# Kernel optimization log

Measured on AMD Instinct MI355X. Metric: run time of the kernel, lower is better.

## Reference

```python
import jax, jax.numpy as jnp
import numpy as np

B, L, G, P, K = 16, 2048, 8, 8, 64
CLAMP = 15.0


def _cdist(x, y):
    # Euclidean pairwise distance: x [..., K, 3], y [..., L, 3] -> [..., K, L]
    x2 = jnp.sum(x * x, axis=-1)[..., :, None]
    y2 = jnp.sum(y * y, axis=-1)[..., None, :]
    xy = jnp.einsum('...kc,...lc->...kl', x, y)
    return jnp.sqrt(jnp.maximum(x2 + y2 - 2.0 * xy, 0.0))


def setup_inputs() -> dict:
    key = jax.random.key(0)
    k1, k2, k3 = jax.random.split(key, 3)
    rng = np.random.default_rng(0)
    # each group: K distinct atom indices; each of the P rows is a permutation of them
    auto = np.empty((G, P, K), dtype=np.int64)
    for g in range(G):
        base = rng.permutation(L)[:K]
        auto[g, 0] = base
        for j in range(1, P):
            auto[g, j] = base[rng.permutation(K)]
    return {
        'x_pred': jax.random.normal(k1, (B, L, 3), jnp.float32),
        'x_native': jax.random.normal(k2, (B, L, 3), jnp.float32),
        'x_native_mask': jax.random.randint(k3, (B, L), 0, 2).astype(bool),
        'automorphs': jnp.asarray(auto),
    }


def reference(x_pred, x_native, x_native_mask, automorphs):
    Bn, Ln = x_pred.shape[0], x_pred.shape[1]
    Kn = automorphs.shape[-1]
    batch_idx = jnp.arange(Bn)
    denom = jnp.asarray(Kn * (Ln - Kn), x_pred.dtype)

    def step(carry, a):
        x_nat, nat_mask = carry
        a0 = a[0]                                           # [K]
        # columns NOT in the symmetry group (the ~mask columns)
        colmask = jnp.ones((Ln,), x_pred.dtype).at[a0].set(0.0)
        d_pred = _cdist(x_pred[:, a0], x_pred)              # [B,K,L]
        gath = x_nat[:, a]                                  # [B,P,K,3]
        d_nat = _cdist(gath, x_nat[:, None])                # [B,P,K,L]
        drms = jnp.minimum(jnp.nan_to_num(jnp.square(d_pred[:, None] - d_nat)), CLAMP)
        drms = jnp.sum(drms * colmask, axis=(-1, -2)) / denom   # [B,P] masked mean
        bestj = jnp.argmin(drms, axis=1)                    # first min <=> strict-< update
        sel = gath[batch_idx, bestj]                        # [B,K,3]
        sel_m = nat_mask[:, a][batch_idx, bestj]            # [B,K]
        x_nat = x_nat.at[:, a0].set(sel)
        nat_mask = nat_mask.at[:, a0].set(sel_m)
        return (x_nat, nat_mask), None

    (x_nat, nat_mask), _ = jax.lax.scan(step, (x_native, x_native_mask), automorphs)
    return x_nat, nat_mask
```

## Files before the change

kernel.cpp:

```cpp
#include <hip/hip_runtime.h>
#include <math.h>

#define Bn 16
#define Ln 2048
#define Gn 8
#define Pn 8
#define Kn 64
#define CLAMP_V 15.0f

#define BPB 32
#define NTH 512
#define NWV (NTH / 64)
#define LPB (Ln / BPB)
#define LPW (LPB / NWV)
#define PK  (Pn * Kn)

#define MAGIC(g) (0x5EED0000u | (unsigned)(g))

typedef unsigned long long ull;

__device__ __forceinline__ float wave_sum64(float x) {
#define DPP_ADD(ctrl) \
    x += __int_as_float(__builtin_amdgcn_update_dpp(0, __float_as_int(x), ctrl, 0xf, 0xf, true))
    DPP_ADD(0x111);
    DPP_ADD(0x112);
    DPP_ADD(0x114);
    DPP_ADD(0x118);
    DPP_ADD(0x142);
    DPP_ADD(0x143);
#undef DPP_ADD
    return x;
}

template <int IMM>
__device__ __forceinline__ float swz_xor(float v) {
    return v + __int_as_float(__builtin_amdgcn_ds_swizzle(__float_as_int(v), IMM));
}
__device__ __forceinline__ ull ld_rlx64(const ull* p) {
    return __hip_atomic_load(p, __ATOMIC_RELAXED, __HIP_MEMORY_SCOPE_AGENT);
}
__device__ __forceinline__ void st_rlx64(ull* p, ull v) {
    __hip_atomic_store(p, v, __ATOMIC_RELAXED, __HIP_MEMORY_SCOPE_AGENT);
}

__global__ __launch_bounds__(NTH, 2) void fused_kernel(
    const float* __restrict__ xpred, const float* __restrict__ xnat,
    const int* __restrict__ mask_in, const int* __restrict__ autom,
    float* __restrict__ out_x, float* __restrict__ out_m,
    ull* __restrict__ part) {

    const int tid  = threadIdx.x;
    const int lane = tid & 63;
    const int wv   = tid >> 6;
    const int b    = blockIdx.x >> 5;
    const int c    = blockIdx.x & (BPB - 1);

    __shared__ float4         s_all[Ln];
    __shared__ unsigned short s_idx[Ln];
    __shared__ unsigned char  s_inv[2][Ln];
    __shared__ float4         s_xp[LPB];
    __shared__ float          s_part[NWV][Pn];

    const float* xpb = xpred + (size_t)b * Ln * 3;
    const float* xnb = xnat  + (size_t)b * Ln * 3;

    for (int l = tid; l < Ln; l += NTH) {
        s_idx[l] = (unsigned short)l;
        s_all[l] = make_float4(xnb[l * 3 + 0], xnb[l * 3 + 1], xnb[l * 3 + 2], 0.0f);
    }
    if (wv == 0) {
        const int l = c * LPB + lane;
        s_xp[lane] = make_float4(xpb[l * 3 + 0], xpb[l * 3 + 1], xpb[l * 3 + 2], 0.0f);
    } else if (wv == 2) {
        s_inv[0][autom[lane]] = (unsigned char)lane;
    }
    int   a0k = autom[lane];
    float px = xpb[a0k * 3 + 0], py = xpb[a0k * 3 + 1], pz = xpb[a0k * 3 + 2];
    __syncthreads();

    #pragma unroll 1
    for (int g = 0; g < Gn; g++) {
        const int* ag  = autom + g * PK;
        const int* ag1 = autom + (g + 1) * PK;
        const int  cur = g & 1, nxt = cur ^ 1;
        ull* pg = part + (size_t)(g * Bn + b) * (BPB * Pn);

        const float4 nk = s_all[s_idx[a0k]];
        int sig[Pn];
        #pragma unroll
        for (int p = 0; p < Pn; p++)
            sig[p] = 4 * (int)s_inv[cur][ag[p * Kn + lane]];
        unsigned short jl[LPW];
        #pragma unroll
        for (int i = 0; i < LPW; i++)
            jl[i] = s_idx[c * LPB + wv * LPW + i];

        float acc[Pn];
        #pragma unroll
        for (int p = 0; p < Pn; p++) acc[p] = 0.0f;

        #pragma unroll 2
        for (int i = 0; i < LPW; i++) {
            const int il = wv * LPW + i;
            const int l  = c * LPB + il;
            if (__ballot(a0k == l)) continue;

            const float4 q = s_xp[il];
            const float4 m = s_all[jl[i]];
            const float dx = px - q.x, dy = py - q.y, dz = pz - q.z;
            const float dp = __builtin_amdgcn_sqrtf(dx * dx + dy * dy + dz * dz);
            const float ex = nk.x - m.x, ey = nk.y - m.y, ez = nk.z - m.z;
            const float dn = __builtin_amdgcn_sqrtf(ex * ex + ey * ey + ez * ez);

            #pragma unroll
            for (int p = 0; p < Pn; p++) {
                const float dns = __int_as_float(
                    __builtin_amdgcn_ds_bpermute(sig[p], __float_as_int(dn)));
                const float e = dp - dns;
                acc[p] += fminf(e * e, CLAMP_V);
            }
        }

        #pragma unroll
        for (int p = 0; p < Pn; p++) {
            const float v = wave_sum64(acc[p]);
            if (lane == 63) s_part[wv][p] = v;
        }
        __syncthreads();

        if (wv == 0) {
            float v = s_part[lane >> 3][lane & 7];
            v = swz_xor<0x201F>(v);
            v = swz_xor<0x401F>(v);
            v += __shfl(v, lane + 32, 64);
            if (lane < 8)
                st_rlx64(&pg[c * Pn + lane],
                         ((ull)MAGIC(g) << 32) | (ull)__float_as_uint(v));
        }

        if (g < Gn - 1) {
            a0k = ag1[lane];
            px = xpb[a0k * 3 + 0]; py = xpb[a0k * 3 + 1]; pz = xpb[a0k * 3 + 2];
            if (wv == 2) s_inv[nxt][ag1[lane]] = (unsigned char)lane;
        }

        if (wv == 0) {
            const unsigned magic = MAGIC(g);
            ull q0 = 0, q1 = 0, q2 = 0, q3 = 0;
            bool r0 = false, r1 = false, r2 = false, r3 = false;
            for (;;) {
                if (!r0) { q0 = ld_rlx64(pg + lane);       r0 = (unsigned)(q0 >> 32) == magic; }
                if (!r1) { q1 = ld_rlx64(pg + lane + 64);  r1 = (unsigned)(q1 >> 32) == magic; }
                if (!r2) { q2 = ld_rlx64(pg + lane + 128); r2 = (unsigned)(q2 >> 32) == magic; }
                if (!r3) { q3 = ld_rlx64(pg + lane + 192); r3 = (unsigned)(q3 >> 32) == magic; }
                if (__ballot(!(r0 && r1 && r2 && r3)) == 0ull) break;
                __builtin_amdgcn_s_sleep(1);
            }
            float v = __uint_as_float((unsigned)q0) + __uint_as_float((unsigned)q1)
                    + __uint_as_float((unsigned)q2) + __uint_as_float((unsigned)q3);
            v = swz_xor<0x201F>(v);
            v = swz_xor<0x401F>(v);
            v += __shfl(v, lane + 32, 64);
            float best = __shfl(v, 0, 64);
            int   bj   = 0;
            #pragma unroll
            for (int p = 1; p < Pn; p++) {
                const float t = __shfl(v, p, 64);
                if (t < best) { best = t; bj = p; }
            }
            const unsigned short oldv = s_idx[ag[bj * Kn + lane]];
            s_idx[ag[lane]] = oldv;
        }
        __syncthreads();
    }

    const int l0 = c * LPB;
    if (tid < LPB * 3) {
        const int ll = tid / 3, coord = tid % 3;
        const int l  = l0 + ll;
        const float4 v = s_all[s_idx[l]];
        out_x[((size_t)b * Ln + l) * 3 + coord] =
            (coord == 0) ? v.x : ((coord == 1) ? v.y : v.z);
    } else if (tid < LPB * 4) {
        const int l = l0 + (tid - LPB * 3);
        const int j = s_idx[l];
        out_m[(size_t)b * Ln + l] = (float)mask_in[(size_t)b * Ln + j];
    }
}

extern "C" void kernel_launch(void* const* d_in, const int* in_sizes, int n_in,
                              void* d_out, int out_size, void* d_ws, size_t ws_size,
                              hipStream_t stream) {
    const float* xpred   = (const float*)d_in[0];
    const float* xnat_in = (const float*)d_in[1];
    const int*   mask_in = (const int*)  d_in[2];
    const int*   autom   = (const int*)  d_in[3];

    float* out_x = (float*)d_out;
    float* out_m = out_x + Bn * Ln * 3;

    ull* part = (ull*)d_ws;

    fused_kernel<<<Bn * BPB, NTH, 0, stream>>>(
        xpred, xnat_in, mask_in, autom, out_x, out_m, part);
}
```

Measured before the change: 116.1 us.

## Speculatively compute next group's distances before cross-block argmin resolves

Computes the next group's masked distance sums before the grid-wide argmin for the current group has been resolved, so the dependent work overlaps the spin-wait on partial sums. Columns and rows whose native coordinates the pending update may change are skipped, then fixed up afterwards. The fix-up covers overlapping group columns and anchor atoms altered by the previous step. It also reformulates the permutation so the predicted distance is permuted via ds_permute-derived indices instead of the native one. This adds substantial complexity, extra LDS state and syncs, and a correctness risk if the speculation bookkeeping is wrong.

Result: slower. 126.3 us (+8.8%).

```diff
diff --git a/kernel.cpp b/kernel.cpp
--- a/kernel.cpp
+++ b/kernel.cpp
@@ -58,8 +58,10 @@
     __shared__ float4         s_all[Ln];
     __shared__ unsigned short s_idx[Ln];
     __shared__ unsigned char  s_inv[2][Ln];
+    __shared__ unsigned char  s_stp[2][Ln];
     __shared__ float4         s_xp[LPB];
     __shared__ float          s_part[NWV][Pn];
+    __shared__ float          s_par2[2][NWV][Pn];
 
     const float* xpb = xpred + (size_t)b * Ln * 3;
     const float* xnb = xnat  + (size_t)b * Ln * 3;
@@ -67,69 +69,103 @@
     for (int l = tid; l < Ln; l += NTH) {
         s_idx[l] = (unsigned short)l;
         s_all[l] = make_float4(xnb[l * 3 + 0], xnb[l * 3 + 1], xnb[l * 3 + 2], 0.0f);
-    }
+        s_stp[0][l] = 0xFF;
+        s_stp[1][l] = 0xFF;
+    }
+    __syncthreads();
+
     if (wv == 0) {
         const int l = c * LPB + lane;
         s_xp[lane] = make_float4(xpb[l * 3 + 0], xpb[l * 3 + 1], xpb[l * 3 + 2], 0.0f);
     } else if (wv == 2) {
         s_inv[0][autom[lane]] = (unsigned char)lane;
-    }
-    int   a0k = autom[lane];
-    float px = xpb[a0k * 3 + 0], py = xpb[a0k * 3 + 1], pz = xpb[a0k * 3 + 2];
+    } else if (wv == 3) {
+        s_stp[0][autom[lane]] = 0;
+    }
+    if (lane < Pn) s_par2[0][wv][lane] = 0.0f;
+
+    int   a0n = autom[lane];
+    int   a0c = a0n;
+    float pxn = xpb[a0n * 3 + 0], pyn = xpb[a0n * 3 + 1], pzn = xpb[a0n * 3 + 2];
     __syncthreads();
+
+    int            sigf[Pn];
+    unsigned short jlv[LPW];
+    float          nsx, nsy, nsz;
+    unsigned       m8n = 0, mg8n = 0;
+    float          acc[Pn];
+    bool           skipme = false;
+
+    auto body = [&](int il, float ncx, float ncy, float ncz, int jidx) {
+        const float4 q = s_xp[il];
+        const float4 m = s_all[jidx];
+        const float2 ux = make_float2(pxn - q.x, ncx - m.x);
+        const float2 uy = make_float2(pyn - q.y, ncy - m.y);
+        const float2 uz = make_float2(pzn - q.z, ncz - m.z);
+        const float2 ss = ux * ux + uy * uy + uz * uz;
+        const float dp = __builtin_amdgcn_sqrtf(ss.x);
+        const float dn = __builtin_amdgcn_sqrtf(ss.y);
+        const int dpi = __float_as_int(dp);
+        const float e0 = dp - dn;
+        acc[0] += fminf(e0 * e0, CLAMP_V);
+        #pragma unroll
+        for (int p = 1; p < Pn; p++) {
+            const float dps = __int_as_float(
+                __builtin_amdgcn_ds_bpermute(sigf[p], dpi));
+            const float e = dps - dn;
+            acc[p] += fminf(e * e, CLAMP_V);
+        }
+    };
+
+    {
+        #pragma unroll
+        for (int p = 0; p < Pn; p++) {
+            const int s = 4 * (int)s_inv[0][autom[p * Kn + lane]];
+            sigf[p] = __builtin_amdgcn_ds_permute(s, 4 * lane);
+        }
+        #pragma unroll
+        for (int i = 0; i < LPW; i++) jlv[i] = s_idx[c * LPB + wv * LPW + i];
+        const float4 nk = s_all[s_idx[a0n]];
+        nsx = nk.x; nsy = nk.y; nsz = nk.z;
+        m8n = 0; mg8n = 0;
+        #pragma unroll
+        for (int i = 0; i < LPW; i++) {
+            const int l = c * LPB + wv * LPW + i;
+            if (__ballot(a0n == l)) m8n |= 1u << i;
+        }
+        #pragma unroll
+        for (int p = 0; p < Pn; p++) acc[p] = 0.0f;
+        #pragma unroll 2
+        for (int i = 0; i < LPW; i++) {
+            if ((m8n >> i) & 1) continue;
+            body(wv * LPW + i, nsx, nsy, nsz, jlv[i]);
+        }
+    }
 
     #pragma unroll 1
     for (int g = 0; g < Gn; g++) {
-        const int* ag  = autom + g * PK;
-        const int* ag1 = autom + (g + 1) * PK;
-        const int  cur = g & 1, nxt = cur ^ 1;
+        const int* ag = autom + g * PK;
         ull* pg = part + (size_t)(g * Bn + b) * (BPB * Pn);
 
-        const float4 nk = s_all[s_idx[a0k]];
-        int sig[Pn];
-        #pragma unroll
-        for (int p = 0; p < Pn; p++)
-            sig[p] = 4 * (int)s_inv[cur][ag[p * Kn + lane]];
-        unsigned short jl[LPW];
-        #pragma unroll
-        for (int i = 0; i < LPW; i++)
-            jl[i] = s_idx[c * LPB + wv * LPW + i];
-
-        float acc[Pn];
-        #pragma unroll
-        for (int p = 0; p < Pn; p++) acc[p] = 0.0f;
-
-        #pragma unroll 2
-        for (int i = 0; i < LPW; i++) {
-            const int il = wv * LPW + i;
-            const int l  = c * LPB + il;
-            if (__ballot(a0k == l)) continue;
-
-            const float4 q = s_xp[il];
-            const float4 m = s_all[jl[i]];
-            const float dx = px - q.x, dy = py - q.y, dz = pz - q.z;
-            const float dp = __builtin_amdgcn_sqrtf(dx * dx + dy * dy + dz * dz);
-            const float ex = nk.x - m.x, ey = nk.y - m.y, ez = nk.z - m.z;
-            const float dn = __builtin_amdgcn_sqrtf(ex * ex + ey * ey + ez * ez);
-
-            #pragma unroll
-            for (int p = 0; p < Pn; p++) {
-                const float dns = __int_as_float(
-                    __builtin_amdgcn_ds_bpermute(sig[p], __float_as_int(dn)));
-                const float e = dp - dns;
-                acc[p] += fminf(e * e, CLAMP_V);
-            }
-        }
+        if (g < Gn - 1) {
+            a0c = a0n;
+            a0n = autom[(g + 1) * PK + lane];
+            pxn = xpb[a0n * 3 + 0]; pyn = xpb[a0n * 3 + 1]; pzn = xpb[a0n * 3 + 2];
+            if (wv == 2)      s_inv[(g + 1) & 1][a0n] = (unsigned char)lane;
+            else if (wv == 3) s_stp[(g + 1) & 1][a0n] = (unsigned char)(g + 1);
+        }
+        if (lane < Pn) s_par2[(g + 1) & 1][wv][lane] = 0.0f;
 
         #pragma unroll
         for (int p = 0; p < Pn; p++) {
-            const float v = wave_sum64(acc[p]);
+            const float v = wave_sum64(skipme ? 0.0f : acc[p]);
             if (lane == 63) s_part[wv][p] = v;
         }
         __syncthreads();
 
         if (wv == 0) {
-            float v = s_part[lane >> 3][lane & 7];
+            float v = s_part[lane >> 3][lane & 7]
+                    + s_par2[g & 1][lane >> 3][lane & 7];
             v = swz_xor<0x201F>(v);
             v = swz_xor<0x401F>(v);
             v += __shfl(v, lane + 32, 64);
@@ -138,10 +174,39 @@
                          ((ull)MAGIC(g) << 32) | (ull)__float_as_uint(v));
         }
 
+        bool skipn = false;
         if (g < Gn - 1) {
-            a0k = ag1[lane];
-            px = xpb[a0k * 3 + 0]; py = xpb[a0k * 3 + 1]; pz = xpb[a0k * 3 + 2];
-            if (wv == 2) s_inv[nxt][ag1[lane]] = (unsigned char)lane;
+            const int* agn = autom + (g + 1) * PK;
+            const unsigned char* inv = s_inv[(g + 1) & 1];
+            #pragma unroll
+            for (int p = 0; p < Pn; p++) {
+                const int s = 4 * (int)inv[agn[p * Kn + lane]];
+                sigf[p] = __builtin_amdgcn_ds_permute(s, 4 * lane);
+            }
+            #pragma unroll
+            for (int i = 0; i < LPW; i++) jlv[i] = s_idx[c * LPB + wv * LPW + i];
+            const float4 nk = s_all[s_idx[a0n]];
+            nsx = nk.x; nsy = nk.y; nsz = nk.z;
+            skipn = (s_stp[g & 1][a0n] == (unsigned char)g);
+            m8n = 0; mg8n = 0;
+            #pragma unroll
+            for (int i = 0; i < LPW; i++) {
+                const int l = c * LPB + wv * LPW + i;
+                if (__ballot(a0n == l)) m8n  |= 1u << i;
+                if (__ballot(a0c == l)) mg8n |= 1u << i;
+            }
+        }
+        __syncthreads();
+
+        if (g < Gn - 1) {
+            const unsigned skipm = m8n | mg8n;
+            #pragma unroll
+            for (int p = 0; p < Pn; p++) acc[p] = 0.0f;
+            #pragma unroll 2
+            for (int i = 0; i < LPW; i++) {
+                if ((skipm >> i) & 1) continue;
+                body(wv * LPW + i, nsx, nsy, nsz, jlv[i]);
+            }
         }
 
         if (wv == 0) {
@@ -172,6 +237,57 @@
             s_idx[ag[lane]] = oldv;
         }
         __syncthreads();
+
+        if (g < Gn - 1) {
+            const float4 nf = s_all[s_idx[a0n]];
+            unsigned cm = mg8n & ~m8n;
+            while (cm) {
+                const int i = __builtin_ctz(cm); cm &= cm - 1;
+                const int j = (int)s_idx[c * LPB + wv * LPW + i];
+                body(wv * LPW + i, nf.x, nf.y, nf.z, j);
+            }
+            const ull D = __ballot(skipn);
+            if (D) {
+                ull Dw = D;
+                const int p_ = lane >> 3, i_ = lane & 7;
+                const float4 q = s_xp[wv * LPW + i_];
+                const float4 M = s_all[s_idx[c * LPB + wv * LPW + i_]];
+                float rp = 0.0f;
+                do {
+                    const int k0 = (int)__builtin_ctzll(Dw); Dw &= Dw - 1;
+                    const int nstar = __shfl(a0n, k0);
+                    const float4 Nn = s_all[s_idx[nstar]];
+                    const unsigned lo =
+                          ((unsigned)__shfl(sigf[0], k0) >> 2)
+                        | (((unsigned)__shfl(sigf[1], k0) >> 2) << 8)
+                        | (((unsigned)__shfl(sigf[2], k0) >> 2) << 16)
+                        | (((unsigned)__shfl(sigf[3], k0) >> 2) << 24);
+                    const unsigned hi =
+                          ((unsigned)__shfl(sigf[4], k0) >> 2)
+                        | (((unsigned)__shfl(sigf[5], k0) >> 2) << 8)
+                        | (((unsigned)__shfl(sigf[6], k0) >> 2) << 16)
+                        | (((unsigned)__shfl(sigf[7], k0) >> 2) << 24);
+                    const unsigned sel = (p_ < 4) ? lo : hi;
+                    const int jp = (int)((sel >> (8 * (p_ & 3))) & 0xFF);
+                    const float cx = __shfl(pxn, jp);
+                    const float cy = __shfl(pyn, jp);
+                    const float cz = __shfl(pzn, jp);
+                    const float dxp = cx - q.x, dyp = cy - q.y, dzp = cz - q.z;
+                    const float dp = __builtin_amdgcn_sqrtf(dxp*dxp + dyp*dyp + dzp*dzp);
+                    const float ex = Nn.x - M.x, ey = Nn.y - M.y, ez = Nn.z - M.z;
+                    const float dn = __builtin_amdgcn_sqrtf(ex*ex + ey*ey + ez*ez);
+                    const float e = dp - dn;
+                    float t = fminf(e * e, CLAMP_V);
+                    if ((m8n >> i_) & 1) t = 0.0f;
+                    rp += t;
+                } while (Dw);
+                rp = swz_xor<0x041F>(rp);
+                rp = swz_xor<0x081F>(rp);
+                rp = swz_xor<0x101F>(rp);
+                if ((lane & 7) == 0) s_par2[(g + 1) & 1][wv][lane >> 3] = rp;
+            }
+        }
+        skipme = skipn;
     }
 
     const int l0 = c * LPB;
```

## Remap blocks per XCD, pack distance math, swap bpermute for LDS row exchange

Applied to the files above, without the earlier changes.

Block indices are remapped so all 32 column-chunks of a batch share the same `bid & 7`. If the hardware deals consecutive blocks round-robin to the 8 XCDs, that puts one batch's cross-block partial-sum handshake on a single XCD and its L2. The inner loop now handles two columns at a time. It uses float2 packed arithmetic for the predicted and native distances, and replaces the per-permutation ds_bpermute with a per-wave LDS row that each lane writes once and then indexes. Permutation 0 reads its own lane directly, and columns in the symmetry group are masked with weights instead of skipping the iteration. This trades cross-lane permute instructions for LDS stores and loads with possible bank conflicts. It also leans on in-order LDS access within a wave for correctness, since there is no barrier between the row write and the reads.

Result: faster. 100.7 us, median of 2 (-13.2%).

```diff
diff --git a/kernel.cpp b/kernel.cpp
--- a/kernel.cpp
+++ b/kernel.cpp
@@ -52,14 +52,16 @@
     const int tid  = threadIdx.x;
     const int lane = tid & 63;
     const int wv   = tid >> 6;
-    const int b    = blockIdx.x >> 5;
-    const int c    = blockIdx.x & (BPB - 1);
+    const int bid  = blockIdx.x;
+    const int b    = (bid & 7) | ((bid >> 8) << 3);
+    const int c    = (bid >> 3) & 31;
 
     __shared__ float4         s_all[Ln];
     __shared__ unsigned short s_idx[Ln];
     __shared__ unsigned char  s_inv[2][Ln];
     __shared__ float4         s_xp[LPB];
     __shared__ float          s_part[NWV][Pn];
+    __shared__ float2         s_dn2[NWV][Kn];
 
     const float* xpb = xpred + (size_t)b * Ln * 3;
     const float* xnb = xnat  + (size_t)b * Ln * 3;
@@ -86,10 +88,14 @@
         ull* pg = part + (size_t)(g * Bn + b) * (BPB * Pn);
 
         const float4 nk = s_all[s_idx[a0k]];
-        int sig[Pn];
+        const float2 cxp = make_float2(px, nk.x);
+        const float2 cyp = make_float2(py, nk.y);
+        const float2 czp = make_float2(pz, nk.z);
+        float2* const dnrow = s_dn2[wv];
+        int sid[Pn];
         #pragma unroll
         for (int p = 0; p < Pn; p++)
-            sig[p] = 4 * (int)s_inv[cur][ag[p * Kn + lane]];
+            sid[p] = (int)s_inv[cur][ag[p * Kn + lane]];
         unsigned short jl[LPW];
         #pragma unroll
         for (int i = 0; i < LPW; i++)
@@ -99,25 +105,64 @@
         #pragma unroll
         for (int p = 0; p < Pn; p++) acc[p] = 0.0f;
 
-        #pragma unroll 2
-        for (int i = 0; i < LPW; i++) {
-            const int il = wv * LPW + i;
-            const int l  = c * LPB + il;
-            if (__ballot(a0k == l)) continue;
-
-            const float4 q = s_xp[il];
-            const float4 m = s_all[jl[i]];
-            const float dx = px - q.x, dy = py - q.y, dz = pz - q.z;
-            const float dp = __builtin_amdgcn_sqrtf(dx * dx + dy * dy + dz * dz);
-            const float ex = nk.x - m.x, ey = nk.y - m.y, ez = nk.z - m.z;
-            const float dn = __builtin_amdgcn_sqrtf(ex * ex + ey * ey + ez * ez);
-
-            #pragma unroll
-            for (int p = 0; p < Pn; p++) {
-                const float dns = __int_as_float(
-                    __builtin_amdgcn_ds_bpermute(sig[p], __float_as_int(dn)));
-                const float e = dp - dns;
-                acc[p] += fminf(e * e, CLAMP_V);
+        #pragma unroll
+        for (int ii = 0; ii < LPW; ii += 2) {
+            const int il0 = wv * LPW + ii;
+            const int l0  = c * LPB + il0;
+            const bool sk0 = __ballot(a0k == l0)     != 0ull;
+            const bool sk1 = __ballot(a0k == l0 + 1) != 0ull;
+            if (sk0 && sk1) continue;
+
+            const float4 q0 = s_xp[il0],      q1 = s_xp[il0 + 1];
+            const float4 m0 = s_all[jl[ii]],  m1 = s_all[jl[ii + 1]];
+            const float2 ux0 = cxp - make_float2(q0.x, m0.x);
+            const float2 uy0 = cyp - make_float2(q0.y, m0.y);
+            const float2 uz0 = czp - make_float2(q0.z, m0.z);
+            const float2 ss0 = ux0 * ux0 + uy0 * uy0 + uz0 * uz0;
+            const float2 ux1 = cxp - make_float2(q1.x, m1.x);
+            const float2 uy1 = cyp - make_float2(q1.y, m1.y);
+            const float2 uz1 = czp - make_float2(q1.z, m1.z);
+            const float2 ss1 = ux1 * ux1 + uy1 * uy1 + uz1 * uz1;
+            const float dp0 = __builtin_amdgcn_sqrtf(ss0.x);
+            const float dn0 = __builtin_amdgcn_sqrtf(ss0.y);
+            const float dp1 = __builtin_amdgcn_sqrtf(ss1.x);
+            const float dn1 = __builtin_amdgcn_sqrtf(ss1.y);
+            dnrow[lane] = make_float2(dn0, dn1);
+            const float2 dpp    = make_float2(dp0, dp1);
+            const float2 dn_own = make_float2(dn0, dn1);
+
+            if (!(sk0 | sk1)) {
+                {
+                    const float2 e = dpp - dn_own;
+                    const float2 s = e * e;
+                    acc[0] += fminf(s.x, CLAMP_V);
+                    acc[0] += fminf(s.y, CLAMP_V);
+                }
+                #pragma unroll
+                for (int p = 1; p < Pn; p++) {
+                    const float2 dns = dnrow[sid[p]];
+                    const float2 e = dpp - dns;
+                    const float2 s = e * e;
+                    acc[p] += fminf(s.x, CLAMP_V);
+                    acc[p] += fminf(s.y, CLAMP_V);
+                }
+            } else {
+                const float w0 = sk0 ? 0.0f : 1.0f;
+                const float w1 = sk1 ? 0.0f : 1.0f;
+                {
+                    const float2 e = dpp - dn_own;
+                    const float2 s = e * e;
+                    acc[0] += fminf(s.x, CLAMP_V) * w0;
+                    acc[0] += fminf(s.y, CLAMP_V) * w1;
+                }
+                #pragma unroll
+                for (int p = 1; p < Pn; p++) {
+                    const float2 dns = dnrow[sid[p]];
+                    const float2 e = dpp - dns;
+                    const float2 s = e * e;
+                    acc[p] += fminf(s.x, CLAMP_V) * w0;
+                    acc[p] += fminf(s.y, CLAMP_V) * w1;
+                }
             }
         }
 
```
